# Kernel optimization log

Hardware: AMD Instinct MI355X
Metric: run time of the kernel (lower is better)

Reference implementation:

```python
import jax, jax.numpy as jnp
import numpy as np


@jax.custom_vjp
def spike(u):
    # Surrogate_BP_Function.forward: u.ge(0).float()
    return (u >= 0).astype(u.dtype)

def _spike_fwd(u):
    return spike(u), u

def _spike_bwd(u, g):
    # backward: g * 0.3 * relu(1 - |u|) * 2
    return (g * 0.6 * jnp.maximum(1.0 - jnp.abs(u), 0.0),)

spike.defvjp(_spike_fwd, _spike_bwd)


def setup_inputs() -> dict:
    key = jax.random.key(0)
    ks = jax.random.split(key, 5)
    B, T, I, H = 64, 512, 256, 512
    x = jax.random.normal(ks[0], (B, T, I), jnp.float32)
    conv1_w = jax.random.normal(ks[1], (H, I, 3), jnp.float32) * 0.1
    conv1_b = jax.random.normal(ks[2], (H,), jnp.float32) * 0.1
    conv2_w = jax.random.normal(ks[3], (H, H, 3), jnp.float32) * 0.1
    conv2_b = jax.random.normal(ks[4], (H,), jnp.float32) * 0.1
    th1 = jnp.ones((), jnp.float32)
    th2 = jnp.ones((), jnp.float32)
    return {"x": x, "conv1_w": conv1_w, "conv1_b": conv1_b,
            "conv2_w": conv2_w, "conv2_b": conv2_b, "th1": th1, "th2": th2}


def reference(x, conv1_w, conv1_b, conv2_w, conv2_b, th1, th2):
    leak = 1.0  # leak_mem from __init__
    # Conv1d(k=3, pad=1) on a length-1 sequence uses only the center tap.
    W1 = conv1_w[:, :, 1]  # [H, I]
    W2 = conv2_w[:, :, 1]  # [H, H]
    B, T, _ = x.shape
    H = W1.shape[0]
    # Precompute input drive for layer 1 (depends only on x[t]).
    z1 = jnp.einsum('bti,hi->bth', x, W1) + conv1_b  # [B, T, H]

    def step(carry, z1_t):
        m1, m2 = carry
        m1 = leak * m1 + z1_t
        thr1 = m1 / th1 - 1.0
        s1 = spike(thr1)
        m1 = m1 - th1 * (thr1 > 0).astype(x.dtype)
        m2 = leak * m2 + s1 @ W2.T + conv2_b
        thr2 = m2 / th2 - 1.0
        s2 = spike(thr2)
        m2 = m2 - th2 * (thr2 > 0).astype(x.dtype)
        return (m1, m2), s2

    init = (jnp.zeros((B, H), x.dtype), jnp.zeros((B, H), x.dtype))
    _, out_t = jax.lax.scan(step, init, jnp.swapaxes(z1, 0, 1))  # [T, B, H]
    return jnp.swapaxes(out_t, 0, 1)  # [B, T, H]
```

## Files before the change

kernel.cpp:

```cpp
#include <hip/hip_runtime.h>

#define BATCH 64
#define TSTEPS 512
#define IDIM 256
#define HDIM 512
#define MROWS (BATCH * TSTEPS)

typedef __attribute__((address_space(1))) const void gvoid;
typedef __attribute__((address_space(3))) void lvoid;

__device__ __forceinline__ void gl2lds16(const void* g, void* l) {
    __builtin_amdgcn_global_load_lds((gvoid*)g, (lvoid*)l, 16, 0, 0);
}

__global__ void extract_weights(const float* __restrict__ c1w,
                                const float* __restrict__ c2w,
                                float* __restrict__ W1T,
                                float* __restrict__ W2T) {
    int tid = blockIdx.x * 256 + threadIdx.x;
    if (tid < IDIM * HDIM) {
        int i = tid >> 9;
        int h = tid & 511;
        W1T[tid] = c1w[(h * IDIM + i) * 3 + 1];
    }
    if (tid < HDIM * HDIM) {
        int h = tid >> 9;
        int j = tid & 511;
        W2T[tid] = c2w[(j * HDIM + h) * 3 + 1];
    }
}

#define BM 128
#define BN 128
#define BK 16

__global__ __launch_bounds__(256, 2) void gemm_f32(const float* __restrict__ A,
                                                   const float* __restrict__ BT,
                                                   const float* __restrict__ bias,
                                                   float* __restrict__ C,
                                                   int K, int addBias) {
    __shared__ __align__(16) float As[BK * BM];
    __shared__ __align__(16) float Bs[BK * BN];

    const int N = HDIM;
    int tid  = threadIdx.x;
    int lane = tid & 63;
    int wave = tid >> 6;
    int row0 = blockIdx.x * BM;
    int col0 = blockIdx.y * BN;
    int wm = (wave >> 1) * 64;
    int wn = (wave & 1) * 64;
    int mbase = wm + (lane >> 3) * 8;
    int nbase = wn + (lane & 7) * 8;

    float acc[8][8];
#pragma unroll
    for (int i = 0; i < 8; i++)
#pragma unroll
        for (int j = 0; j < 8; j++) acc[i][j] = 0.0f;

    int ar = tid >> 1;
    int ak = (tid & 1) * 8;
    const float* ap = A + (size_t)(row0 + ar) * K + ak;

    const char* bp = (const char*)(BT + (size_t)(tid >> 5) * N + col0) + (tid & 31) * 16;
    char* bld = (char*)Bs + tid * 16;
    const size_t bRow8 = (size_t)8 * N * sizeof(float);

    for (int k0 = 0; k0 < K; k0 += BK) {
        gl2lds16(bp, bld);
        gl2lds16(bp + bRow8, bld + 4096);
        float4 a0 = *(const float4*)(ap);
        float4 a1 = *(const float4*)(ap + 4);
        ap += BK;
        bp += (size_t)BK * N * sizeof(float);
        As[(ak + 0) * BM + ar] = a0.x;
        As[(ak + 1) * BM + ar] = a0.y;
        As[(ak + 2) * BM + ar] = a0.z;
        As[(ak + 3) * BM + ar] = a0.w;
        As[(ak + 4) * BM + ar] = a1.x;
        As[(ak + 5) * BM + ar] = a1.y;
        As[(ak + 6) * BM + ar] = a1.z;
        As[(ak + 7) * BM + ar] = a1.w;
        __syncthreads();

#pragma unroll
        for (int k = 0; k < BK; k++) {
            float4 av0 = *(const float4*)&As[k * BM + mbase];
            float4 av1 = *(const float4*)&As[k * BM + mbase + 4];
            float4 bv0 = *(const float4*)&Bs[k * BN + nbase];
            float4 bv1 = *(const float4*)&Bs[k * BN + nbase + 4];
            float a8[8] = {av0.x, av0.y, av0.z, av0.w, av1.x, av1.y, av1.z, av1.w};
            float b8[8] = {bv0.x, bv0.y, bv0.z, bv0.w, bv1.x, bv1.y, bv1.z, bv1.w};
#pragma unroll
            for (int i = 0; i < 8; i++)
#pragma unroll
                for (int j = 0; j < 8; j++)
                    acc[i][j] = fmaf(a8[i], b8[j], acc[i][j]);
        }
        __syncthreads();
    }

    float bb[8];
#pragma unroll
    for (int j = 0; j < 8; j++)
        bb[j] = addBias ? bias[col0 + nbase + j] : 0.0f;
#pragma unroll
    for (int i = 0; i < 8; i++) {
        int row = row0 + mbase + i;
        float4* cp = (float4*)&C[(size_t)row * N + col0 + nbase];
        cp[0] = (float4){acc[i][0] + bb[0], acc[i][1] + bb[1],
                         acc[i][2] + bb[2], acc[i][3] + bb[3]};
        cp[1] = (float4){acc[i][4] + bb[4], acc[i][5] + bb[5],
                         acc[i][6] + bb[6], acc[i][7] + bb[7]};
    }
}

__global__ void lif_scan1(const float* __restrict__ z1,
                          unsigned long long* __restrict__ masks,
                          const float* __restrict__ th_p) {
    int gtid = blockIdx.x * blockDim.x + threadIdx.x;
    int b = gtid >> 9;
    int h = gtid & 511;
    int lane = threadIdx.x & 63;
    int w = h >> 6;
    float th = *th_p;
    const float* zp = z1 + (size_t)b * TSTEPS * HDIM + h;
    unsigned long long* mp = masks + (size_t)b * TSTEPS * 8 + w;
    float m = 0.0f;
    float bufA[16], bufB[16];
#pragma unroll
    for (int i = 0; i < 16; i++) bufA[i] = zp[(size_t)i * HDIM];
    for (int t0 = 0; t0 < TSTEPS; t0 += 32) {
#pragma unroll
        for (int i = 0; i < 16; i++) bufB[i] = zp[(size_t)(t0 + 16 + i) * HDIM];
        {
#pragma unroll
            for (int i = 0; i < 16; i++) {
                m += bufA[i];
                float thr = m / th - 1.0f;
                unsigned long long bal = __ballot(thr >= 0.0f);
                if (lane == 0) mp[(size_t)(t0 + i) * 8] = bal;
                if (thr > 0.0f) m -= th;
            }
        }
        if (t0 + 32 < TSTEPS) {
#pragma unroll
            for (int i = 0; i < 16; i++) bufA[i] = zp[(size_t)(t0 + 32 + i) * HDIM];
        }
        {
#pragma unroll
            for (int i = 0; i < 16; i++) {
                m += bufB[i];
                float thr = m / th - 1.0f;
                unsigned long long bal = __ballot(thr >= 0.0f);
                if (lane == 0) mp[(size_t)(t0 + 16 + i) * 8] = bal;
                if (thr > 0.0f) m -= th;
            }
        }
    }
}

__global__ __launch_bounds__(256) void spmm_spikes(
        const unsigned long long* __restrict__ masks,
        const float* __restrict__ W2T,
        float* __restrict__ C) {
    int lane = threadIdx.x & 63;
    int wave = threadIdx.x >> 6;
    int m = blockIdx.x * 4 + wave;
    const unsigned long long* mrow = masks + (size_t)m * 8;

    float4 s0 = {0.0f, 0.0f, 0.0f, 0.0f};
    float4 s1 = {0.0f, 0.0f, 0.0f, 0.0f};

    for (int c = 0; c < 8; c++) {
        unsigned long long mraw = mrow[c];
        unsigned int lo = __builtin_amdgcn_readfirstlane((unsigned int)mraw);
        unsigned int hi = __builtin_amdgcn_readfirstlane((unsigned int)(mraw >> 32));
        unsigned long long mk = ((unsigned long long)hi << 32) | lo;
        const float* wc = W2T + ((size_t)(c << 6)) * HDIM + lane * 8;
        while (mk) {
            int k = __builtin_ctzll(mk);
            mk &= mk - 1;
            const float4* wp = (const float4*)(wc + (size_t)k * HDIM);
            float4 w0 = wp[0];
            float4 w1 = wp[1];
            s0.x += w0.x; s0.y += w0.y; s0.z += w0.z; s0.w += w0.w;
            s1.x += w1.x; s1.y += w1.y; s1.z += w1.z; s1.w += w1.w;
        }
    }

    float4* cp = (float4*)(C + (size_t)m * HDIM + lane * 8);
    cp[0] = s0;
    cp[1] = s1;
}

__global__ void lif_scan2(const float* __restrict__ raw,
                          const float* __restrict__ b2,
                          const float* __restrict__ th_p,
                          float* __restrict__ out) {
    int gtid = blockIdx.x * blockDim.x + threadIdx.x;
    int b = gtid >> 9;
    int j = gtid & 511;
    float th = *th_p;
    float bias = b2[j];
    const float* rp = raw + (size_t)b * TSTEPS * HDIM + j;
    float* op = out + (size_t)b * TSTEPS * HDIM + j;
    float m = 0.0f;
    float bufA[16], bufB[16];
#pragma unroll
    for (int i = 0; i < 16; i++) bufA[i] = rp[(size_t)i * HDIM];
    for (int t0 = 0; t0 < TSTEPS; t0 += 32) {
#pragma unroll
        for (int i = 0; i < 16; i++) bufB[i] = rp[(size_t)(t0 + 16 + i) * HDIM];
        {
            float ss[16];
#pragma unroll
            for (int i = 0; i < 16; i++) {
                m = (m + bufA[i]) + bias;
                float thr = m / th - 1.0f;
                ss[i] = (thr >= 0.0f) ? 1.0f : 0.0f;
                if (thr > 0.0f) m -= th;
            }
#pragma unroll
            for (int i = 0; i < 16; i++) op[(size_t)(t0 + i) * HDIM] = ss[i];
        }
        if (t0 + 32 < TSTEPS) {
#pragma unroll
            for (int i = 0; i < 16; i++) bufA[i] = rp[(size_t)(t0 + 32 + i) * HDIM];
        }
        {
            float ss[16];
#pragma unroll
            for (int i = 0; i < 16; i++) {
                m = (m + bufB[i]) + bias;
                float thr = m / th - 1.0f;
                ss[i] = (thr >= 0.0f) ? 1.0f : 0.0f;
                if (thr > 0.0f) m -= th;
            }
#pragma unroll
            for (int i = 0; i < 16; i++) op[(size_t)(t0 + 16 + i) * HDIM] = ss[i];
        }
    }
}

extern "C" void kernel_launch(void* const* d_in, const int* in_sizes, int n_in,
                              void* d_out, int out_size, void* d_ws, size_t ws_size,
                              hipStream_t stream) {
    const float* x    = (const float*)d_in[0];
    const float* c1w  = (const float*)d_in[1];
    const float* c1b  = (const float*)d_in[2];
    const float* c2w  = (const float*)d_in[3];
    const float* c2b  = (const float*)d_in[4];
    const float* th1  = (const float*)d_in[5];
    const float* th2  = (const float*)d_in[6];
    float* out = (float*)d_out;

    float* W1T  = (float*)d_ws;
    float* W2T  = W1T + IDIM * HDIM;
    float* bufA = W2T + HDIM * HDIM;
    unsigned long long* masks = (unsigned long long*)(bufA + (size_t)MROWS * HDIM);

    extract_weights<<<(HDIM * HDIM + 255) / 256, 256, 0, stream>>>(c1w, c2w, W1T, W2T);

    {
        dim3 grid(MROWS / BM, HDIM / BN);
        gemm_f32<<<grid, 256, 0, stream>>>(x, W1T, c1b, bufA, IDIM, 1);
    }

    lif_scan1<<<MROWS / 64, 64, 0, stream>>>(bufA, masks, th1);

    spmm_spikes<<<MROWS / 4, 256, 0, stream>>>(masks, W2T, bufA);

    lif_scan2<<<MROWS / 64, 64, 0, stream>>>(bufA, c2b, th2, out);
}
```

Baseline: 396.1 us.

## Compact spike indices and double-buffer W2 rows into LDS in spike SpMM

The spike SpMM kernel now builds a compacted list of active spike indices in LDS per row, padded to multiples of four with a zero weight row. It streams four W2T rows at a time into a double-buffered LDS stage using global_load_lds, overlapping the next fetch with accumulation of the current one. This replaces the serial per-bit dependent global loads, aiming to hide memory latency. In exchange it uses one-wave blocks (launch_bounds 64,1), an extra LDS round trip, and hand-placed waitcnt/sched barriers that limit occupancy.

```diff
diff --git a/kernel.cpp b/kernel.cpp
--- a/kernel.cpp
+++ b/kernel.cpp
@@ -5,6 +5,7 @@
 #define IDIM 256
 #define HDIM 512
 #define MROWS (BATCH * TSTEPS)
+#define KZ HDIM
 
 typedef __attribute__((address_space(1))) const void gvoid;
 typedef __attribute__((address_space(3))) void lvoid;
@@ -27,6 +28,9 @@
         int h = tid >> 9;
         int j = tid & 511;
         W2T[tid] = c2w[(j * HDIM + h) * 3 + 1];
+    }
+    if (tid < HDIM) {
+        W2T[HDIM * HDIM + tid] = 0.0f;
     }
 }
 
@@ -161,36 +165,88 @@
     }
 }
 
-__global__ __launch_bounds__(256) void spmm_spikes(
+#define CH 4
+
+__global__ __launch_bounds__(64, 1) void spmm_spikes(
         const unsigned long long* __restrict__ masks,
         const float* __restrict__ W2T,
         float* __restrict__ C) {
-    int lane = threadIdx.x & 63;
-    int wave = threadIdx.x >> 6;
-    int m = blockIdx.x * 4 + wave;
+    __shared__ __align__(16) float stage[2][CH][HDIM];
+    __shared__ __align__(16) unsigned short klist[520];
+    int lane = threadIdx.x;
+    int m = blockIdx.x;
     const unsigned long long* mrow = masks + (size_t)m * 8;
+
+    unsigned long long wv[8];
+#pragma unroll
+    for (int c = 0; c < 8; c++) wv[c] = mrow[c];
+
+    int cnt = 0;
+#pragma unroll
+    for (int c = 0; c < 8; c++) {
+        unsigned long long bal = wv[c];
+        int below = (int)__popcll(bal & ((1ull << lane) - 1ull));
+        if ((bal >> lane) & 1ull)
+            klist[cnt + below] = (unsigned short)((c << 6) | lane);
+        cnt += (int)__popcll(bal);
+    }
+    int pad = (-cnt) & (CH - 1);
+    if (lane < pad) klist[cnt + lane] = (unsigned short)KZ;
+    cnt += pad;
+    cnt = __builtin_amdgcn_readfirstlane(cnt);
+    int nch = cnt >> 2;
 
     float4 s0 = {0.0f, 0.0f, 0.0f, 0.0f};
     float4 s1 = {0.0f, 0.0f, 0.0f, 0.0f};
 
-    for (int c = 0; c < 8; c++) {
-        unsigned long long mraw = mrow[c];
-        unsigned int lo = __builtin_amdgcn_readfirstlane((unsigned int)mraw);
-        unsigned int hi = __builtin_amdgcn_readfirstlane((unsigned int)(mraw >> 32));
-        unsigned long long mk = ((unsigned long long)hi << 32) | lo;
-        const float* wc = W2T + ((size_t)(c << 6)) * HDIM + lane * 8;
-        while (mk) {
-            int k = __builtin_ctzll(mk);
-            mk &= mk - 1;
-            const float4* wp = (const float4*)(wc + (size_t)k * HDIM);
-            float4 w0 = wp[0];
-            float4 w1 = wp[1];
-            s0.x += w0.x; s0.y += w0.y; s0.z += w0.z; s0.w += w0.w;
-            s1.x += w1.x; s1.y += w1.y; s1.z += w1.z; s1.w += w1.w;
-        }
-    }
-
-    float4* cp = (float4*)(C + (size_t)m * HDIM + lane * 8);
+#define STAGE(buf, ci)                                                      \
+    {                                                                       \
+        ushort4 kq_ = *(const ushort4*)(klist + ((ci) << 2));               \
+        const float* g0_ = W2T + (size_t)kq_.x * HDIM + (lane << 2);        \
+        const float* g1_ = W2T + (size_t)kq_.y * HDIM + (lane << 2);        \
+        const float* g2_ = W2T + (size_t)kq_.z * HDIM + (lane << 2);        \
+        const float* g3_ = W2T + (size_t)kq_.w * HDIM + (lane << 2);        \
+        float* l_ = &stage[buf][0][0] + (lane << 2);                        \
+        gl2lds16(g0_,       l_);                                            \
+        gl2lds16(g0_ + 256, l_ + 256);                                      \
+        gl2lds16(g1_,       l_ + 512);                                      \
+        gl2lds16(g1_ + 256, l_ + 768);                                      \
+        gl2lds16(g2_,       l_ + 1024);                                     \
+        gl2lds16(g2_ + 256, l_ + 1280);                                     \
+        gl2lds16(g3_,       l_ + 1536);                                     \
+        gl2lds16(g3_ + 256, l_ + 1792);                                     \
+    }
+
+    if (nch > 0) {
+        asm volatile("s_waitcnt vmcnt(0)" ::: "memory");
+        __builtin_amdgcn_sched_barrier(0);
+        STAGE(0, 0);
+        int cur = 0;
+        for (int c = 0; c < nch; c++) {
+            if (c + 1 < nch) {
+                STAGE(cur ^ 1, c + 1);
+                __builtin_amdgcn_sched_barrier(0);
+                asm volatile("s_waitcnt vmcnt(8)" ::: "memory");
+            } else {
+                __builtin_amdgcn_sched_barrier(0);
+                asm volatile("s_waitcnt vmcnt(0)" ::: "memory");
+            }
+            __builtin_amdgcn_sched_barrier(0);
+            const float* base = &stage[cur][0][0] + (lane << 3);
+#pragma unroll
+            for (int q = 0; q < CH; q++) {
+                float4 w0 = *(const float4*)(base + q * HDIM);
+                float4 w1 = *(const float4*)(base + q * HDIM + 4);
+                s0.x += w0.x; s0.y += w0.y; s0.z += w0.z; s0.w += w0.w;
+                s1.x += w1.x; s1.y += w1.y; s1.z += w1.z; s1.w += w1.w;
+            }
+            __builtin_amdgcn_sched_barrier(0);
+            cur ^= 1;
+        }
+    }
+#undef STAGE
+
+    float4* cp = (float4*)(C + (size_t)m * HDIM + (lane << 3));
     cp[0] = s0;
     cp[1] = s1;
 }
@@ -258,7 +314,7 @@
 
     float* W1T  = (float*)d_ws;
     float* W2T  = W1T + IDIM * HDIM;
-    float* bufA = W2T + HDIM * HDIM;
+    float* bufA = W2T + (HDIM + 1) * HDIM;
     unsigned long long* masks = (unsigned long long*)(bufA + (size_t)MROWS * HDIM);
 
     extract_weights<<<(HDIM * HDIM + 255) / 256, 256, 0, stream>>>(c1w, c2w, W1T, W2T);
@@ -270,7 +326,7 @@
 
     lif_scan1<<<MROWS / 64, 64, 0, stream>>>(bufA, masks, th1);
 
-    spmm_spikes<<<MROWS / 4, 256, 0, stream>>>(masks, W2T, bufA);
+    spmm_spikes<<<MROWS, 64, 0, stream>>>(masks, W2T, bufA);
 
     lif_scan2<<<MROWS / 64, 64, 0, stream>>>(bufA, c2b, th2, out);
 }
```

After: 381.0 us. -3.8%, faster.

## Compact spike indices into LDS and software-pipeline sparse row gathers

Applied to the files above, without the earlier changes.

The spike-SpMM kernel now builds a per-wave list of active column indices in LDS using ballot masks and popcount prefix sums, padded to a multiple of four with a zero row appended to W2T. It then walks this list with a four-deep software pipeline, issuing row loads ahead of the accumulations and using sched barriers to keep them in that order. Lanes now read interleaved float4 columns (lane*4 and +256) instead of eight consecutive floats, which gives coalesced loads. The aim is to hide global-load latency that the serial ctz loop exposed, at the cost of extra LDS traffic, padding work and a larger workspace.

```diff
diff --git a/kernel.cpp b/kernel.cpp
--- a/kernel.cpp
+++ b/kernel.cpp
@@ -5,6 +5,7 @@
 #define IDIM 256
 #define HDIM 512
 #define MROWS (BATCH * TSTEPS)
+#define KZ HDIM
 
 typedef __attribute__((address_space(1))) const void gvoid;
 typedef __attribute__((address_space(3))) void lvoid;
@@ -27,6 +28,9 @@
         int h = tid >> 9;
         int j = tid & 511;
         W2T[tid] = c2w[(j * HDIM + h) * 3 + 1];
+    }
+    if (tid < HDIM) {
+        W2T[HDIM * HDIM + tid] = 0.0f;
     }
 }
 
@@ -161,38 +165,75 @@
     }
 }
 
+#define SB __builtin_amdgcn_sched_barrier(0)
+
+#define LOADQ(X0, X1, kk)                                                   \
+    {                                                                       \
+        const float* p_ = W2T + (size_t)(kk) * HDIM + (lane << 2);          \
+        X0 = *(const float4*)(p_);                                          \
+        X1 = *(const float4*)(p_ + 256);                                    \
+    }
+
+#define ACCQ(X0, X1)                                                        \
+    s0.x += X0.x; s0.y += X0.y; s0.z += X0.z; s0.w += X0.w;                 \
+    s1.x += X1.x; s1.y += X1.y; s1.z += X1.z; s1.w += X1.w;
+
 __global__ __launch_bounds__(256) void spmm_spikes(
         const unsigned long long* __restrict__ masks,
         const float* __restrict__ W2T,
         float* __restrict__ C) {
+    __shared__ __align__(16) unsigned short klist[4][520];
     int lane = threadIdx.x & 63;
     int wave = threadIdx.x >> 6;
     int m = blockIdx.x * 4 + wave;
     const unsigned long long* mrow = masks + (size_t)m * 8;
+    unsigned short* klw = klist[wave];
+
+    unsigned long long wv[8];
+#pragma unroll
+    for (int c = 0; c < 8; c++) wv[c] = mrow[c];
+
+    int cnt = 0;
+#pragma unroll
+    for (int c = 0; c < 8; c++) {
+        unsigned long long bal = wv[c];
+        int below = (int)__popcll(bal & ((1ull << lane) - 1ull));
+        if ((bal >> lane) & 1ull)
+            klw[cnt + below] = (unsigned short)((c << 6) | lane);
+        cnt += (int)__popcll(bal);
+    }
+    int pad = (-cnt) & 3;
+    if (lane < pad) klw[cnt + lane] = (unsigned short)KZ;
+    cnt += pad;
+    cnt = __builtin_amdgcn_readfirstlane(cnt);
+    if (lane < 4) klw[cnt + lane] = (unsigned short)KZ;
 
     float4 s0 = {0.0f, 0.0f, 0.0f, 0.0f};
     float4 s1 = {0.0f, 0.0f, 0.0f, 0.0f};
 
-    for (int c = 0; c < 8; c++) {
-        unsigned long long mraw = mrow[c];
-        unsigned int lo = __builtin_amdgcn_readfirstlane((unsigned int)mraw);
-        unsigned int hi = __builtin_amdgcn_readfirstlane((unsigned int)(mraw >> 32));
-        unsigned long long mk = ((unsigned long long)hi << 32) | lo;
-        const float* wc = W2T + ((size_t)(c << 6)) * HDIM + lane * 8;
-        while (mk) {
-            int k = __builtin_ctzll(mk);
-            mk &= mk - 1;
-            const float4* wp = (const float4*)(wc + (size_t)k * HDIM);
-            float4 w0 = wp[0];
-            float4 w1 = wp[1];
-            s0.x += w0.x; s0.y += w0.y; s0.z += w0.z; s0.w += w0.w;
-            s1.x += w1.x; s1.y += w1.y; s1.z += w1.z; s1.w += w1.w;
-        }
-    }
-
-    float4* cp = (float4*)(C + (size_t)m * HDIM + lane * 8);
-    cp[0] = s0;
-    cp[1] = s1;
+    if (cnt > 0) {
+        float4 a0, a1, b0, b1, c0, c1, d0, d1;
+        ushort4 qc = *(const ushort4*)(klw);
+        LOADQ(a0, a1, qc.x);
+        LOADQ(b0, b1, qc.y);
+        LOADQ(c0, c1, qc.z);
+        for (int i = 0; i < cnt; i += 4) {
+            ushort4 qn = *(const ushort4*)(klw + i + 4);
+            LOADQ(d0, d1, qc.w); SB;
+            ACCQ(a0, a1); SB;
+            LOADQ(a0, a1, qn.x); SB;
+            ACCQ(b0, b1); SB;
+            LOADQ(b0, b1, qn.y); SB;
+            ACCQ(c0, c1); SB;
+            LOADQ(c0, c1, qn.z); SB;
+            ACCQ(d0, d1); SB;
+            qc = qn;
+        }
+    }
+
+    float* crow = C + (size_t)m * HDIM;
+    *(float4*)(crow + (lane << 2))       = s0;
+    *(float4*)(crow + 256 + (lane << 2)) = s1;
 }
 
 __global__ void lif_scan2(const float* __restrict__ raw,
@@ -258,7 +299,7 @@
 
     float* W1T  = (float*)d_ws;
     float* W2T  = W1T + IDIM * HDIM;
-    float* bufA = W2T + HDIM * HDIM;
+    float* bufA = W2T + (HDIM + 1) * HDIM;
     unsigned long long* masks = (unsigned long long*)(bufA + (size_t)MROWS * HDIM);
 
     extract_weights<<<(HDIM * HDIM + 255) / 256, 256, 0, stream>>>(c1w, c2w, W1T, W2T);
```

Measured after the change: 404.9 us. +2.2%, slower.
